# Performance work log

Measured on AMD Instinct MI355X. Metric: run time of the kernel, lower is better.

## Reference

```python
import jax, jax.numpy as jnp
import numpy as np

L = 2      # num_layers
H = 1024   # hidden_size
E = 1024   # embed_size (== H so per-layer weights stack)
T = 4096   # sequence length


def setup_inputs() -> dict:
    key = jax.random.key(0)
    ks = jax.random.split(key, 10)
    scale = 1.0 / np.sqrt(H)  # PyTorch LSTM default init is U(-1/sqrt(H), 1/sqrt(H))
    return {
        "s1": jax.random.normal(ks[0], (T, E), jnp.float32),
        "s2": jax.random.normal(ks[1], (T, E), jnp.float32),
        # initHiddenCell(): randn initial states, one pair per branch; batch=1 squeezed
        "h1_0": jax.random.normal(ks[2], (L, H), jnp.float32),
        "c1_0": jax.random.normal(ks[3], (L, H), jnp.float32),
        "h2_0": jax.random.normal(ks[4], (L, H), jnp.float32),
        "c2_0": jax.random.normal(ks[5], (L, H), jnp.float32),
        # LSTM params, PyTorch layout: gates stacked as [i, f, g, o] along 4H
        "W_ih": jax.random.uniform(ks[6], (L, 4 * H, E), jnp.float32, -scale, scale),
        "W_hh": jax.random.uniform(ks[7], (L, 4 * H, H), jnp.float32, -scale, scale),
        "b_ih": jax.random.uniform(ks[8], (L, 4 * H), jnp.float32, -scale, scale),
        "b_hh": jax.random.uniform(ks[9], (L, 4 * H), jnp.float32, -scale, scale),
    }


def _run_lstm(seq, h0, c0, W_ih, W_hh, b_ih, b_hh):
    """Multi-layer LSTM over [T, E] sequence; returns last-step top-layer output [H]."""
    x = seq
    for l in range(L):
        Wi, Wh = W_ih[l], W_hh[l]
        b = b_ih[l] + b_hh[l]

        def step(carry, xt, Wi=Wi, Wh=Wh, b=b):
            h, c = carry
            g = Wi @ xt + Wh @ h + b           # [4H]
            i, f, gg, o = jnp.split(g, 4)
            c = jax.nn.sigmoid(f) * c + jax.nn.sigmoid(i) * jnp.tanh(gg)
            h = jax.nn.sigmoid(o) * jnp.tanh(c)
            return (h, c), h

        (_, _), x = jax.lax.scan(step, (h0[l], c0[l]), x)  # x: [T, H]
    return x[-1]


def reference(s1, s2, h1_0, c1_0, h2_0, c2_0, W_ih, W_hh, b_ih, b_hh):
    o1 = _run_lstm(s1, h1_0, c1_0, W_ih, W_hh, b_ih, b_hh)
    o2 = _run_lstm(s2, h2_0, c2_0, W_ih, W_hh, b_ih, b_hh)
    # 5 * exp(-||o1 - o2||_1)
    return 5.0 * jnp.exp(-jnp.sum(jnp.abs(o1 - o2)))
```

## Files before the change

### kernel.cpp

```cpp
#include <hip/hip_runtime.h>
#include <math.h>
#include <stdint.h>

#define T_SEQ 4096

__device__ __forceinline__ float sigm(float x) { return 1.0f / (1.0f + expf(-x)); }

__device__ __forceinline__ void wave0_barrier(uint32_t* bar, uint32_t ord, int t) {
    if (t == 0)
        __hip_atomic_fetch_add(bar + ((blockIdx.x >> 4) << 5), 1u,
                               __ATOMIC_RELAXED, __HIP_MEMORY_SCOPE_AGENT);
    if (blockIdx.x == 0) {
        if (t < 16) {
            uint32_t* cnt = bar + (t << 5);
            while (__hip_atomic_load(cnt, __ATOMIC_RELAXED, __HIP_MEMORY_SCOPE_AGENT) < (ord << 4))
                __builtin_amdgcn_s_sleep(1);
            __hip_atomic_store(bar + 512 + (t << 5), ord,
                               __ATOMIC_RELAXED, __HIP_MEMORY_SCOPE_AGENT);
        }
    } else if (t == 0) {
        uint32_t* rel = bar + 512 + ((blockIdx.x >> 4) << 5);
        while (__hip_atomic_load(rel, __ATOMIC_RELAXED, __HIP_MEMORY_SCOPE_AGENT) < ord)
            __builtin_amdgcn_s_sleep(1);
    }
}

__global__ void __launch_bounds__(256) gemm_nt_bias(
    const float* __restrict__ A0, const float* __restrict__ A1,
    const float* __restrict__ B,
    const float* __restrict__ bias1, const float* __restrict__ bias2,
    float* __restrict__ C)
{
    const int t  = threadIdx.x;
    const int tx = t & 15, ty = t >> 4;
    const int n0 = blockIdx.x * 128, m0 = blockIdx.y * 128;
    const float* Ab = (m0 < 4096) ? A0 : A1;
    const int ml0 = (m0 < 4096) ? m0 : (m0 - 4096);

    __shared__ float As[16 * 140];
    __shared__ float Bs[16 * 140];

    const int lr = t >> 1;
    const int lh = t & 1;
    const int pw = lr + ((lr >> 5) << 2);
    const int pa = ty * 8 + ((ty >> 2) << 2);
    const int pb = tx * 8 + ((tx >> 2) << 2);

    float acc[8][8];
#pragma unroll
    for (int i = 0; i < 8; ++i)
#pragma unroll
        for (int j = 0; j < 8; ++j) acc[i][j] = 0.f;

    for (int k0 = 0; k0 < 1024; k0 += 16) {
        const float* ap = Ab + (size_t)(ml0 + lr) * 1024 + k0 + lh * 8;
        float4 av0 = *(const float4*)ap;
        float4 av1 = *(const float4*)(ap + 4);
        const float* bp = B + (size_t)(n0 + lr) * 1024 + k0 + lh * 8;
        float4 bv0 = *(const float4*)bp;
        float4 bv1 = *(const float4*)(bp + 4);

        __syncthreads();
        const int kb = lh * 8;
        As[(kb + 0) * 140 + pw] = av0.x;  As[(kb + 1) * 140 + pw] = av0.y;
        As[(kb + 2) * 140 + pw] = av0.z;  As[(kb + 3) * 140 + pw] = av0.w;
        As[(kb + 4) * 140 + pw] = av1.x;  As[(kb + 5) * 140 + pw] = av1.y;
        As[(kb + 6) * 140 + pw] = av1.z;  As[(kb + 7) * 140 + pw] = av1.w;
        Bs[(kb + 0) * 140 + pw] = bv0.x;  Bs[(kb + 1) * 140 + pw] = bv0.y;
        Bs[(kb + 2) * 140 + pw] = bv0.z;  Bs[(kb + 3) * 140 + pw] = bv0.w;
        Bs[(kb + 4) * 140 + pw] = bv1.x;  Bs[(kb + 5) * 140 + pw] = bv1.y;
        Bs[(kb + 6) * 140 + pw] = bv1.z;  Bs[(kb + 7) * 140 + pw] = bv1.w;
        __syncthreads();

#pragma unroll
        for (int kk = 0; kk < 16; ++kk) {
            float4 a0 = *(const float4*)&As[kk * 140 + pa];
            float4 a1 = *(const float4*)&As[kk * 140 + pa + 4];
            float4 b0 = *(const float4*)&Bs[kk * 140 + pb];
            float4 b1 = *(const float4*)&Bs[kk * 140 + pb + 4];
            float a[8]  = {a0.x, a0.y, a0.z, a0.w, a1.x, a1.y, a1.z, a1.w};
            float bb[8] = {b0.x, b0.y, b0.z, b0.w, b1.x, b1.y, b1.z, b1.w};
#pragma unroll
            for (int i = 0; i < 8; ++i)
#pragma unroll
                for (int j = 0; j < 8; ++j)
                    acc[i][j] = fmaf(a[i], bb[j], acc[i][j]);
        }
    }

    const int gcol  = n0 >> 10;
    const int qbase = (n0 & 1023) + tx * 8;
    const int j0 = n0 + tx * 8;
    float bsv[8];
#pragma unroll
    for (int j = 0; j < 8; ++j) bsv[j] = bias1[j0 + j] + bias2[j0 + j];
#pragma unroll
    for (int i = 0; i < 8; ++i) {
        const size_t rowoff = (size_t)(m0 + ty * 8 + i) * 4096;
#pragma unroll
        for (int jj = 0; jj < 8; ++jj) {
            const int q = qbase + jj;
            C[rowoff + ((q >> 2) << 4) + (gcol << 2) + (q & 3)] = acc[i][jj] + bsv[jj];
        }
    }
}

__global__ void __launch_bounds__(256, 1) lstm_fused(
    const float* __restrict__ W_hh,
    const float* __restrict__ W_ih,
    const float* __restrict__ b_ih,
    const float* __restrict__ b_hh,
    const float* __restrict__ G,
    const float* __restrict__ h1_0, const float* __restrict__ c1_0,
    const float* __restrict__ h2_0, const float* __restrict__ c2_0,
    float* __restrict__ hbuf,
    float* __restrict__ o_out,
    uint32_t* __restrict__ bar)
{
    const int b = blockIdx.x, t = threadIdx.x;
    const int row = t & 15, slice = t >> 4;
    const int gate = row >> 2, uoff = row & 3;
    const int j_glob = gate * 1024 + b * 4 + uoff;

    float4 w0[16], w1h[16], w1i[16];
    {
        const float* r0 = W_hh + (size_t)j_glob * 1024 + slice * 64;
        const float* r1 = W_hh + 4194304ull + (size_t)j_glob * 1024 + slice * 64;
        const float* r2 = W_ih + 4194304ull + (size_t)j_glob * 1024 + slice * 64;
#pragma unroll
        for (int m = 0; m < 16; ++m) {
            const int o = ((m + slice) & 15) << 2;
            w0[m]  = *(const float4*)(r0 + o);
            w1h[m] = *(const float4*)(r1 + o);
            w1i[m] = *(const float4*)(r2 + o);
        }
    }

    __shared__ float hs[4096];
    __shared__ float red[4][4][16];
    __shared__ float bl1s[16];

    float creg = 0.f;
    if (t < 16) {
        const int layer = t >> 3, br = (t >> 2) & 1, u = t & 3;
        const float* cc = br ? c2_0 : c1_0;
        const float* hh = br ? h2_0 : h1_0;
        creg = cc[layer * 1024 + b * 4 + u];
        const float hinit = hh[layer * 1024 + b * 4 + u];
        __hip_atomic_store(&hbuf[4096 + layer * 2048 + br * 1024 + b * 4 + u],
                           hinit, __ATOMIC_RELAXED, __HIP_MEMORY_SCOPE_AGENT);
        if (layer == 1)
            __hip_atomic_store(&hbuf[2048 + br * 1024 + b * 4 + u],
                               hinit, __ATOMIC_RELAXED, __HIP_MEMORY_SCOPE_AGENT);
    }
    if (t >= 32 && t < 48) {
        const int rr = t & 15;
        const int jj = 4096 + (rr >> 2) * 1024 + b * 4 + (rr & 3);
        bl1s[rr] = b_ih[jj] + b_hh[jj];
    }
    if (t < 64) {
        asm volatile("s_waitcnt vmcnt(0)" ::: "memory");
        wave0_barrier(bar, 1u, t);
    }
    __syncthreads();

    for (int tick = 0; tick <= T_SEQ; ++tick) {
        {
            const float* src = hbuf + ((tick + 1) & 1) * 4096;
            float v[16];
#pragma unroll
            for (int r = 0; r < 16; ++r)
                v[r] = __hip_atomic_load(src + t + r * 256, __ATOMIC_RELAXED,
                                         __HIP_MEMORY_SCOPE_AGENT);
#pragma unroll
            for (int r = 0; r < 16; ++r)
                hs[t + r * 256] = v[r];
        }
        float gpre = 0.f;
        if (t < 32) {
            const int br = t >> 4, rr = t & 15;
            const int st = (tick < T_SEQ) ? tick : (T_SEQ - 1);
            gpre = G[((size_t)br * T_SEQ + st) * 4096 + b * 16 + rr];
        }
        __syncthreads();

        float a00 = 0.f, a01 = 0.f, a10 = 0.f, a11 = 0.f;
        const float4* H00 = (const float4*)hs;
        const float4* H01 = (const float4*)(hs + 1024);
        const float4* H10 = (const float4*)(hs + 2048);
        const float4* H11 = (const float4*)(hs + 3072);
#pragma unroll
        for (int m = 0; m < 16; ++m) {
            const int ci = (slice << 4) + ((m + slice) & 15);
            const float4 x0 = H00[ci], x1 = H01[ci];
            const float4 y0 = H10[ci], y1 = H11[ci];
            a00 = fmaf(w0[m].x, x0.x, a00); a00 = fmaf(w0[m].y, x0.y, a00);
            a00 = fmaf(w0[m].z, x0.z, a00); a00 = fmaf(w0[m].w, x0.w, a00);
            a01 = fmaf(w0[m].x, x1.x, a01); a01 = fmaf(w0[m].y, x1.y, a01);
            a01 = fmaf(w0[m].z, x1.z, a01); a01 = fmaf(w0[m].w, x1.w, a01);
            a10 = fmaf(w1i[m].x, x0.x, a10); a10 = fmaf(w1i[m].y, x0.y, a10);
            a10 = fmaf(w1i[m].z, x0.z, a10); a10 = fmaf(w1i[m].w, x0.w, a10);
            a10 = fmaf(w1h[m].x, y0.x, a10); a10 = fmaf(w1h[m].y, y0.y, a10);
            a10 = fmaf(w1h[m].z, y0.z, a10); a10 = fmaf(w1h[m].w, y0.w, a10);
            a11 = fmaf(w1i[m].x, x1.x, a11); a11 = fmaf(w1i[m].y, x1.y, a11);
            a11 = fmaf(w1i[m].z, x1.z, a11); a11 = fmaf(w1i[m].w, x1.w, a11);
            a11 = fmaf(w1h[m].x, y1.x, a11); a11 = fmaf(w1h[m].y, y1.y, a11);
            a11 = fmaf(w1h[m].z, y1.z, a11); a11 = fmaf(w1h[m].w, y1.w, a11);
        }
        a00 += __shfl_xor(a00, 16); a00 += __shfl_xor(a00, 32);
        a01 += __shfl_xor(a01, 16); a01 += __shfl_xor(a01, 32);
        a10 += __shfl_xor(a10, 16); a10 += __shfl_xor(a10, 32);
        a11 += __shfl_xor(a11, 16); a11 += __shfl_xor(a11, 32);
        const int wv = t >> 6, lane = t & 63;
        if (lane < 16) {
            red[wv][0][lane] = a00; red[wv][1][lane] = a01;
            red[wv][2][lane] = a10; red[wv][3][lane] = a11;
        }
        __syncthreads();

        if (t < 64) {
            const int lb = t >> 4, rr = t & 15;
            float s = red[0][lb][rr] + red[1][lb][rr] + red[2][lb][rr] + red[3][lb][rr];
            s += (lb < 2) ? gpre : bl1s[rr];
            const int src0 = ((t >> 2) << 4) + (t & 3);
            const float gi = __shfl(s, src0);
            const float gf = __shfl(s, src0 + 4);
            const float gg = __shfl(s, src0 + 8);
            const float go = __shfl(s, src0 + 12);
            if (t < 16) {
                const int layer = t >> 3, br = (t >> 2) & 1, u = t & 3;
                const bool active = (layer == 0) ? (tick < T_SEQ) : (tick >= 1);
                if (active) {
                    const float c = sigm(gf) * creg + sigm(gi) * tanhf(gg);
                    const float h = sigm(go) * tanhf(c);
                    creg = c;
                    __hip_atomic_store(&hbuf[(tick & 1) * 4096 + layer * 2048 + br * 1024 + b * 4 + u],
                                       h, __ATOMIC_RELAXED, __HIP_MEMORY_SCOPE_AGENT);
                    if (layer == 1 && tick == T_SEQ)
                        o_out[br * 1024 + b * 4 + u] = h;
                }
            }
            if (tick < T_SEQ) {
                asm volatile("s_waitcnt vmcnt(0)" ::: "memory");
                wave0_barrier(bar, (uint32_t)tick + 2u, t);
            }
        }
        __syncthreads();
    }
}

__global__ void __launch_bounds__(256) dist_kernel(const float* __restrict__ o,
                                                   float* __restrict__ out)
{
    int t = threadIdx.x;
    float s = 0.f;
    for (int i = t; i < 1024; i += 256) s += fabsf(o[i] - o[i + 1024]);
#pragma unroll
    for (int off = 1; off < 64; off <<= 1) s += __shfl_xor(s, off);
    __shared__ float r[4];
    if ((t & 63) == 0) r[t >> 6] = s;
    __syncthreads();
    if (t == 0) out[0] = 5.0f * expf(-(r[0] + r[1] + r[2] + r[3]));
}

extern "C" void kernel_launch(void* const* d_in, const int* in_sizes, int n_in,
                              void* d_out, int out_size, void* d_ws, size_t ws_size,
                              hipStream_t stream) {
    const float* s1   = (const float*)d_in[0];
    const float* s2   = (const float*)d_in[1];
    const float* h1_0 = (const float*)d_in[2];
    const float* c1_0 = (const float*)d_in[3];
    const float* h2_0 = (const float*)d_in[4];
    const float* c2_0 = (const float*)d_in[5];
    const float* W_ih = (const float*)d_in[6];
    const float* W_hh = (const float*)d_in[7];
    const float* b_ih = (const float*)d_in[8];
    const float* b_hh = (const float*)d_in[9];

    uint8_t* w8 = (uint8_t*)d_ws;
    uint32_t* bar  = (uint32_t*)(w8);
    float* hbuf  = (float*)(w8 + 8192);
    float* o_out = (float*)(w8 + 8192 + 32768);
    float* G     = (float*)(w8 + 65536);

    hipMemsetAsync(d_ws, 0, 8192, stream);

    dim3 ggrid(32, 64);
    gemm_nt_bias<<<ggrid, 256, 0, stream>>>(s1, s2, W_ih, b_ih, b_hh, G);

    {
        const float* whh = W_hh; const float* wih = W_ih;
        const float* bi = b_ih;  const float* bh = b_hh;
        const float* gg = G;
        const float* h1p = h1_0; const float* c1p = c1_0;
        const float* h2p = h2_0; const float* c2p = c2_0;
        float* hb = hbuf; float* oo = o_out; uint32_t* br = bar;
        void* args[] = { &whh, &wih, &bi, &bh, &gg,
                         &h1p, &c1p, &h2p, &c2p, &hb, &oo, &br };
        hipLaunchCooperativeKernel(lstm_fused, dim3(256), dim3(256), args, 0, stream);
    }

    dist_kernel<<<1, 256, 0, stream>>>(o_out, (float*)d_out);
}
```

Before: 16.73 ms.

## Replace two-level grid barrier with all-block polling and reorganize h buffer layout

```diff
diff --git a/kernel.cpp b/kernel.cpp
--- a/kernel.cpp
+++ b/kernel.cpp
@@ -10,17 +10,10 @@
     if (t == 0)
         __hip_atomic_fetch_add(bar + ((blockIdx.x >> 4) << 5), 1u,
                                __ATOMIC_RELAXED, __HIP_MEMORY_SCOPE_AGENT);
-    if (blockIdx.x == 0) {
-        if (t < 16) {
-            uint32_t* cnt = bar + (t << 5);
-            while (__hip_atomic_load(cnt, __ATOMIC_RELAXED, __HIP_MEMORY_SCOPE_AGENT) < (ord << 4))
-                __builtin_amdgcn_s_sleep(1);
-            __hip_atomic_store(bar + 512 + (t << 5), ord,
-                               __ATOMIC_RELAXED, __HIP_MEMORY_SCOPE_AGENT);
-        }
-    } else if (t == 0) {
-        uint32_t* rel = bar + 512 + ((blockIdx.x >> 4) << 5);
-        while (__hip_atomic_load(rel, __ATOMIC_RELAXED, __HIP_MEMORY_SCOPE_AGENT) < ord)
+    if (t < 16) {
+        const uint32_t target = ord << 4;
+        uint32_t* cnt = bar + (t << 5);
+        while (__hip_atomic_load(cnt, __ATOMIC_RELAXED, __HIP_MEMORY_SCOPE_AGENT) < target)
             __builtin_amdgcn_s_sleep(1);
     }
 }
@@ -142,16 +135,16 @@
 
     float creg = 0.f;
     if (t < 16) {
-        const int layer = t >> 3, br = (t >> 2) & 1, u = t & 3;
+        const int layer = t >> 3, br = (t >> 2) & 1;
         const float* cc = br ? c2_0 : c1_0;
         const float* hh = br ? h2_0 : h1_0;
-        creg = cc[layer * 1024 + b * 4 + u];
-        const float hinit = hh[layer * 1024 + b * 4 + u];
-        __hip_atomic_store(&hbuf[4096 + layer * 2048 + br * 1024 + b * 4 + u],
-                           hinit, __ATOMIC_RELAXED, __HIP_MEMORY_SCOPE_AGENT);
+        creg = cc[layer * 1024 + b * 4 + (t & 3)];
+        const float hinit = hh[layer * 1024 + b * 4 + (t & 3)];
+        __hip_atomic_store(&hbuf[4096 + b * 16 + t], hinit,
+                           __ATOMIC_RELAXED, __HIP_MEMORY_SCOPE_AGENT);
         if (layer == 1)
-            __hip_atomic_store(&hbuf[2048 + br * 1024 + b * 4 + u],
-                               hinit, __ATOMIC_RELAXED, __HIP_MEMORY_SCOPE_AGENT);
+            __hip_atomic_store(&hbuf[b * 16 + t], hinit,
+                               __ATOMIC_RELAXED, __HIP_MEMORY_SCOPE_AGENT);
     }
     if (t >= 32 && t < 48) {
         const int rr = t & 15;
@@ -164,17 +157,21 @@
     }
     __syncthreads();
 
+    const int q_st = t >> 3, k_st = t & 7;
+    const int dst_base = (k_st >> 1) * 512 + q_st * 2 + (k_st & 1);
+
     for (int tick = 0; tick <= T_SEQ; ++tick) {
         {
-            const float* src = hbuf + ((tick + 1) & 1) * 4096;
-            float v[16];
-#pragma unroll
-            for (int r = 0; r < 16; ++r)
-                v[r] = __hip_atomic_load(src + t + r * 256, __ATOMIC_RELAXED,
+            const uint64_t* src64 = (const uint64_t*)(hbuf + ((tick + 1) & 1) * 4096);
+            uint64_t v[8];
+#pragma unroll
+            for (int r = 0; r < 8; ++r)
+                v[r] = __hip_atomic_load(src64 + r * 256 + t, __ATOMIC_RELAXED,
                                          __HIP_MEMORY_SCOPE_AGENT);
-#pragma unroll
-            for (int r = 0; r < 16; ++r)
-                hs[t + r * 256] = v[r];
+            uint64_t* hs64 = (uint64_t*)hs;
+#pragma unroll
+            for (int r = 0; r < 8; ++r)
+                hs64[dst_base + r * 64] = v[r];
         }
         float gpre = 0.f;
         if (t < 32) {
@@ -205,7 +202,7 @@
             a11 = fmaf(w1i[m].x, x1.x, a11); a11 = fmaf(w1i[m].y, x1.y, a11);
             a11 = fmaf(w1i[m].z, x1.z, a11); a11 = fmaf(w1i[m].w, x1.w, a11);
             a11 = fmaf(w1h[m].x, y1.x, a11); a11 = fmaf(w1h[m].y, y1.y, a11);
-            a11 = fmaf(w1h[m].z, y1.z, a11); a11 = fmaf(w1h[m].w, y1.w, a11);
+            a11 = fmaf(w1h[m].w, y1.w, a11); a11 = fmaf(w1h[m].z, y1.z, a11);
         }
         a00 += __shfl_xor(a00, 16); a00 += __shfl_xor(a00, 32);
         a01 += __shfl_xor(a01, 16); a01 += __shfl_xor(a01, 32);
@@ -234,8 +231,8 @@
                     const float c = sigm(gf) * creg + sigm(gi) * tanhf(gg);
                     const float h = sigm(go) * tanhf(c);
                     creg = c;
-                    __hip_atomic_store(&hbuf[(tick & 1) * 4096 + layer * 2048 + br * 1024 + b * 4 + u],
-                                       h, __ATOMIC_RELAXED, __HIP_MEMORY_SCOPE_AGENT);
+                    __hip_atomic_store(&hbuf[(tick & 1) * 4096 + b * 16 + t], h,
+                                       __ATOMIC_RELAXED, __HIP_MEMORY_SCOPE_AGENT);
                     if (layer == 1 && tick == T_SEQ)
                         o_out[br * 1024 + b * 4 + u] = h;
                 }
```

After: 24.36 ms. 45.6% more time.
